# Performance work log

Measured on AMD Instinct MI355X. Metric: run time of the kernel, lower is better.

Reference implementation:

```python
import jax, jax.numpy as jnp
import numpy as np

N_DRUG = 25000
N_DIS = 25000
N = N_DRUG + N_DIS
E = 800000
D_IN = 128
D_OUT = 128


def setup_inputs() -> dict:
    key = jax.random.key(0)
    k1, k2, k3, k4, k5, k6 = jax.random.split(key, 6)
    drug_f = jax.random.normal(k1, (N_DRUG, D_IN), dtype=jnp.float32)
    disease_f = jax.random.normal(k2, (N_DIS, D_IN), dtype=jnp.float32)
    rows = jax.random.randint(k3, (E,), 0, N, dtype=jnp.int64)
    cols = jax.random.randint(k4, (E,), 0, N, dtype=jnp.int64)
    # xavier_uniform_ equivalent for [D_IN, D_OUT]
    limit = float(np.sqrt(6.0 / (D_IN + D_OUT)))
    drug_w = jax.random.uniform(k5, (D_IN, D_OUT), minval=-limit, maxval=limit, dtype=jnp.float32)
    disease_w = jax.random.uniform(k6, (D_IN, D_OUT), minval=-limit, maxval=limit, dtype=jnp.float32)
    return {"drug_f": drug_f, "disease_f": disease_f, "drug_w": drug_w,
            "disease_w": disease_w, "rows": rows, "cols": cols}


def reference(drug_f, disease_f, drug_w, disease_w, rows, cols):
    # per-type linear projection
    drug_h = drug_f @ drug_w          # [n_drug, D_OUT]
    dis_h = disease_f @ disease_w     # [n_dis,  D_OUT]
    node_f = jnp.concatenate([drug_h, dis_h], axis=0)  # [N, D_OUT]
    # row-sum degrees of the (unit-valued) sparse adjacency, clamped at 1
    deg = jax.ops.segment_sum(jnp.ones((rows.shape[0],), node_f.dtype), rows,
                              num_segments=N)
    norm = jnp.clip(deg, 1.0, None) ** -0.5           # [N]
    # symmetric norm: norm * (A @ (norm * x)); SpMM as gather + segment_sum
    node_f = node_f * norm[:, None]
    msgs = node_f[cols]                               # [E, D_OUT]
    node_f = jax.ops.segment_sum(msgs, rows, num_segments=N)
    node_f = node_f * norm[:, None]
    return node_f
```

## Files before the change

### kernel.cpp

```cpp
#include <hip/hip_runtime.h>
#include <hip/hip_bf16.h>

#define D 128
#define CAP 64
#define BINSH 7
#define NSHARD 8
#define NCHUNK 384

typedef short short8 __attribute__((ext_vector_type(8)));
typedef unsigned short ushort8 __attribute__((ext_vector_type(8)));
typedef float f32x4  __attribute__((ext_vector_type(4)));

__device__ __forceinline__ short f2bf(float x) {
    __hip_bfloat16 b = __float2bfloat16(x);
    return *reinterpret_cast<short*>(&b);
}
__device__ __forceinline__ float bf2f(unsigned short u) {
    return __uint_as_float((unsigned)u << 16);
}

__global__ __launch_bounds__(256) void part_proj_kernel(
    const int* __restrict__ rows, const int* __restrict__ cols,
    int* __restrict__ counts, unsigned int* __restrict__ payload,
    int E, int nbin, int nparts, int pe, int capseg,
    const float* __restrict__ f0, const float* __restrict__ f1,
    const float* __restrict__ w0, const float* __restrict__ w1,
    __hip_bfloat16* __restrict__ h,
    int n0, int n1, int nb0) {

    __shared__ short8 Wl[2048];
    int b = blockIdx.x;
    int t = threadIdx.x;

    if (b < nparts) {
        int* cur = (int*)&Wl[0];
        for (int i = t; i < nbin; i += 256) cur[i] = 0;
        __syncthreads();
        int lo = b * pe;
        int hi = lo + pe; if (hi > E) hi = E;
        for (int i = lo + t; i < hi; i += 256) {
            int r = rows[i];
            int c = cols[i];
            int bn = r >> BINSH;
            int p = atomicAdd(&cur[bn], 1);
            if (p < capseg)
                payload[((size_t)bn * nparts + b) * capseg + p] =
                    ((unsigned)r << 16) | (unsigned)(c & 0xffff);
        }
        __syncthreads();
        for (int i = t; i < nbin; i += 256) {
            int c = cur[i]; if (c > capseg) c = capseg;
            counts[(size_t)i * nparts + b] = c;
        }
        return;
    }

    int pb = b - nparts;
    int type = (pb >= nb0) ? 1 : 0;
    const float* f = type ? f1 : f0;
    const float* W = type ? w1 : w0;
    int lbase = (type ? (pb - nb0) : pb) * 64;
    int nloc  = type ? n1 : n0;
    int goff  = type ? n0 : 0;

    for (int i = t; i < 2048; i += 256) {
        int lane = i & 63, ts = i >> 6;
        int s = ts & 3, tt = ts >> 2;
        int n = tt * 16 + (lane & 15);
        int kbase = s * 32 + (lane >> 4) * 8;
        short8 v;
        #pragma unroll
        for (int j = 0; j < 8; ++j)
            v[j] = f2bf(W[(size_t)(kbase + j) * D + n]);
        Wl[i] = v;
    }
    __syncthreads();

    int wave = t >> 6;
    int lane = t & 63;
    int m  = lane & 15;
    int kg = lane >> 4;
    int wrow = lbase + wave * 16;

    int arow = wrow + m;
    int arc = (arow < nloc) ? arow : (nloc - 1);
    const float* fr = f + (size_t)arc * D + kg * 8;
    short8 A[4];
    #pragma unroll
    for (int s = 0; s < 4; ++s) {
        float4 x = *(const float4*)(fr + s * 32);
        float4 y = *(const float4*)(fr + s * 32 + 4);
        short8 a;
        a[0] = f2bf(x.x); a[1] = f2bf(x.y); a[2] = f2bf(x.z); a[3] = f2bf(x.w);
        a[4] = f2bf(y.x); a[5] = f2bf(y.y); a[6] = f2bf(y.z); a[7] = f2bf(y.w);
        A[s] = a;
    }

    #pragma unroll
    for (int tt = 0; tt < 8; ++tt) {
        f32x4 acc = {0.f, 0.f, 0.f, 0.f};
        #pragma unroll
        for (int s = 0; s < 4; ++s)
            acc = __builtin_amdgcn_mfma_f32_16x16x32_bf16(A[s], Wl[(tt * 4 + s) * 64 + lane], acc, 0, 0, 0);
        #pragma unroll
        for (int r = 0; r < 4; ++r) {
            int grow = wrow + kg * 4 + r;
            if (grow < nloc)
                h[(size_t)(goff + grow) * D + tt * 16 + m] = __float2bfloat16(acc[r]);
        }
    }
}

__global__ __launch_bounds__(256) void binfill_kernel(const unsigned int* __restrict__ payload,
                                                      const int* __restrict__ counts,
                                                      unsigned short* __restrict__ bucket,
                                                      int* __restrict__ cnt,
                                                      float* __restrict__ normf,
                                                      int nparts, int capseg, int N) {
    __shared__ int rc[128];
    int b = blockIdx.x;
    int t = threadIdx.x;
    if (t < 128) rc[t] = 0;
    __syncthreads();
    if (t < nparts) {
        int cntc = counts[(size_t)b * nparts + t];
        if (cntc > capseg) cntc = capseg;
        const unsigned int* seg = payload + ((size_t)b * nparts + t) * capseg;
        for (int p = 0; p < cntc; ++p) {
            unsigned pay = seg[p];
            int rl = (pay >> 16) & 127;
            int q = atomicAdd(&rc[rl], 1);
            if (q < CAP)
                bucket[(size_t)((b << BINSH) | rl) * CAP + q] = (unsigned short)(pay & 0xffff);
        }
    }
    __syncthreads();
    if (t < 128) {
        int r = (b << BINSH) | t;
        if (r < N) {
            int c = rc[t];
            cnt[r] = c;
            normf[r] = rsqrtf((float)(c < 1 ? 1 : c));
        }
    }
}

__global__ __launch_bounds__(256) void agg_kernel(const int* __restrict__ cnt,
                                                  const float* __restrict__ normf,
                                                  const unsigned short* __restrict__ bucket,
                                                  const __hip_bfloat16* __restrict__ h,
                                                  float* __restrict__ out, int n) {
    int wave = threadIdx.x >> 6;
    int lane = threadIdx.x & 63;
    int r = blockIdx.x * 4 + wave;
    if (r >= n) return;
    int d = cnt[r]; if (d > CAP) d = CAP;
    int s = r * CAP;

    int col = (int)bucket[s + lane];
    int cs  = (lane < d) ? col : 0;
    float wl = (lane < d) ? normf[cs] : 0.f;

    int g  = lane >> 4;
    int sl = lane & 15;

    float acc[8] = {0.f,0.f,0.f,0.f,0.f,0.f,0.f,0.f};
    int j = 0;
    for (; j + 16 <= d; j += 16) {
        int e0 = j + g, e1 = j + 4 + g, e2 = j + 8 + g, e3 = j + 12 + g;
        float w0 = __shfl(wl, e0), w1 = __shfl(wl, e1), w2 = __shfl(wl, e2), w3 = __shfl(wl, e3);
        int   c0 = __shfl(cs, e0), c1 = __shfl(cs, e1), c2 = __shfl(cs, e2), c3 = __shfl(cs, e3);
        ushort8 v0 = *(const ushort8*)&h[(size_t)c0 * D + sl * 8];
        ushort8 v1 = *(const ushort8*)&h[(size_t)c1 * D + sl * 8];
        ushort8 v2 = *(const ushort8*)&h[(size_t)c2 * D + sl * 8];
        ushort8 v3 = *(const ushort8*)&h[(size_t)c3 * D + sl * 8];
        #pragma unroll
        for (int k = 0; k < 8; ++k)
            acc[k] += (w0 * bf2f(v0[k]) + w1 * bf2f(v1[k])) + (w2 * bf2f(v2[k]) + w3 * bf2f(v3[k]));
    }
    for (; j + 8 <= d; j += 8) {
        int e0 = j + g, e1 = j + 4 + g;
        float w0 = __shfl(wl, e0), w1 = __shfl(wl, e1);
        int   c0 = __shfl(cs, e0), c1 = __shfl(cs, e1);
        ushort8 v0 = *(const ushort8*)&h[(size_t)c0 * D + sl * 8];
        ushort8 v1 = *(const ushort8*)&h[(size_t)c1 * D + sl * 8];
        #pragma unroll
        for (int k = 0; k < 8; ++k)
            acc[k] += w0 * bf2f(v0[k]) + w1 * bf2f(v1[k]);
    }
    for (; j < d; j += 4) {
        int e = j + g;
        float we = __shfl(wl, e & 63); if (e >= d) we = 0.f;
        int   ce = __shfl(cs, e & 63);
        ushort8 v = *(const ushort8*)&h[(size_t)ce * D + sl * 8];
        #pragma unroll
        for (int k = 0; k < 8; ++k)
            acc[k] += we * bf2f(v[k]);
    }
    #pragma unroll
    for (int k = 0; k < 8; ++k) {
        acc[k] += __shfl_xor(acc[k], 16);
        acc[k] += __shfl_xor(acc[k], 32);
    }
    if (g == 0) {
        float nr = normf[r];
        float* po = &out[(size_t)r * D + sl * 8];
        *(float4*)po       = make_float4(acc[0]*nr, acc[1]*nr, acc[2]*nr, acc[3]*nr);
        *(float4*)(po + 4) = make_float4(acc[4]*nr, acc[5]*nr, acc[6]*nr, acc[7]*nr);
    }
}

__global__ void zero_cnt_kernel(int* __restrict__ cnt, int N) {
    int i = blockIdx.x * 256 + threadIdx.x;
    if (i < N) cnt[i] = 0;
}

__global__ __launch_bounds__(256) void fill_shard_kernel(const int* __restrict__ rows,
                                                         const int* __restrict__ cols,
                                                         int* __restrict__ cnt,
                                                         unsigned short* __restrict__ bucket,
                                                         int E, int shsz, int ch) {
    int s     = blockIdx.x & (NSHARD - 1);
    int chunk = blockIdx.x >> 3;
    int lo = chunk * ch;
    int hi = lo + ch; if (hi > E) hi = E;
    int rlo = s * shsz;
    for (int i = lo + (int)threadIdx.x; i < hi; i += 256) {
        int r = rows[i];
        if ((unsigned)(r - rlo) < (unsigned)shsz) {
            int p = atomicAdd(&cnt[r], 1);
            if (p < CAP) bucket[(size_t)r * CAP + p] = (unsigned short)cols[i];
        }
    }
}

__global__ void norm_from_cnt_kernel(const int* __restrict__ cnt, float* __restrict__ normf, int N) {
    int i = blockIdx.x * 256 + threadIdx.x;
    if (i < N) { int c = cnt[i]; normf[i] = rsqrtf((float)(c < 1 ? 1 : c)); }
}

extern "C" void kernel_launch(void* const* d_in, const int* in_sizes, int n_in,
                              void* d_out, int out_size, void* d_ws, size_t ws_size,
                              hipStream_t stream) {
    const float* drug_f    = (const float*)d_in[0];
    const float* disease_f = (const float*)d_in[1];
    const float* drug_w    = (const float*)d_in[2];
    const float* disease_w = (const float*)d_in[3];
    const int*   rows      = (const int*)d_in[4];
    const int*   cols      = (const int*)d_in[5];
    float* out = (float*)d_out;

    int n_drug = in_sizes[0] / D;
    int n_dis  = in_sizes[1] / D;
    int N = n_drug + n_dis;
    int E = in_sizes[4];
    (void)out_size; (void)n_in;

    char* ws = (char*)d_ws;
    size_t off = 0;
    auto alloc = [&](size_t bytes) { void* p = ws + off; off = (off + bytes + 255) & ~(size_t)255; return p; };

    int*            cnt      = (int*)alloc(sizeof(int) * N);
    float*          normf    = (float*)alloc(sizeof(float) * N);
    __hip_bfloat16* h_raw    = (__hip_bfloat16*)alloc(sizeof(__hip_bfloat16) * (size_t)N * D);
    unsigned short* bucket   = (unsigned short*)alloc((size_t)N * CAP * sizeof(unsigned short));

    int nb0 = (n_drug + 63) / 64;
    int nb1 = (n_dis + 63) / 64;

    int nbin = (N + (1 << BINSH) - 1) >> BINSH;
    int pe = (E + 255) / 256;
    if (pe < 4096) pe = 4096;
    int nparts = (E + pe - 1) / pe;
    int capseg = ((pe / nbin) * 3 + 31) & ~15;

    size_t sort_need = off
        + ((sizeof(int) * (size_t)nbin * nparts + 255) & ~(size_t)255)
        + ((sizeof(unsigned int) * (size_t)nbin * nparts * capseg + 255) & ~(size_t)255);

    if (ws_size >= sort_need && nbin <= 512 && nparts <= 256) {
        int*          counts  = (int*)alloc(sizeof(int) * (size_t)nbin * nparts);
        unsigned int* payload = (unsigned int*)alloc(sizeof(unsigned int) * (size_t)nbin * nparts * capseg);

        part_proj_kernel<<<nparts + nb0 + nb1, 256, 0, stream>>>(
            rows, cols, counts, payload, E, nbin, nparts, pe, capseg,
            drug_f, disease_f, drug_w, disease_w, h_raw, n_drug, n_dis, nb0);
        binfill_kernel<<<nbin, 256, 0, stream>>>(payload, counts, bucket, cnt, normf,
                                                 nparts, capseg, N);
        agg_kernel<<<(N + 3) / 4, 256, 0, stream>>>(cnt, normf, bucket, h_raw, out, N);
    } else {
        int shsz = (N + NSHARD - 1) / NSHARD;
        int ch   = (E + NCHUNK - 1) / NCHUNK;

        zero_cnt_kernel<<<(N + 255) / 256, 256, 0, stream>>>(cnt, N);
        fill_shard_kernel<<<NCHUNK * NSHARD, 256, 0, stream>>>(rows, cols, cnt, bucket, E, shsz, ch);
        norm_from_cnt_kernel<<<(N + 255) / 256, 256, 0, stream>>>(cnt, normf, N);
        part_proj_kernel<<<nb0 + nb1, 256, 0, stream>>>(
            rows, cols, (int*)nullptr, (unsigned int*)nullptr, E, nbin, 0, pe, capseg,
            drug_f, disease_f, drug_w, disease_w, h_raw, n_drug, n_dis, nb0);
        agg_kernel<<<(N + 3) / 4, 256, 0, stream>>>(cnt, normf, bucket, h_raw, out, N);
    }
}
```

Before: 64.15 us.

## Replace capped per-bin payload segments with exact local counting sort per partition

Each partition block now builds a histogram of row bins in shared memory, prefix-scans it, scatters the packed (row,col) pairs into a shared staging buffer in bin order, and writes them out contiguously with vectorized stores. It also records per-bin offsets. binfill then reads exact [start,end) ranges instead of fixed-capacity segments. This removes the capseg overflow truncation and the sparse, oversized payload layout, and makes global writes coalesced. The cost is an extra pass over rows plus a block-wide scan in each partition block.

```diff
diff --git a/kernel.cpp b/kernel.cpp
--- a/kernel.cpp
+++ b/kernel.cpp
@@ -4,6 +4,7 @@
 #define D 128
 #define CAP 64
 #define BINSH 7
+#define PE 4096
 #define NSHARD 8
 #define NCHUNK 384
 
@@ -21,8 +22,9 @@
 
 __global__ __launch_bounds__(256) void part_proj_kernel(
     const int* __restrict__ rows, const int* __restrict__ cols,
-    int* __restrict__ counts, unsigned int* __restrict__ payload,
-    int E, int nbin, int nparts, int pe, int capseg,
+    int* __restrict__ base_m,
+    unsigned int* __restrict__ payload,
+    int E, int nbin, int nparts,
     const float* __restrict__ f0, const float* __restrict__ f1,
     const float* __restrict__ w0, const float* __restrict__ w1,
     __hip_bfloat16* __restrict__ h,
@@ -33,25 +35,51 @@
     int t = threadIdx.x;
 
     if (b < nparts) {
-        int* cur = (int*)&Wl[0];
-        for (int i = t; i < nbin; i += 256) cur[i] = 0;
-        __syncthreads();
-        int lo = b * pe;
-        int hi = lo + pe; if (hi > E) hi = E;
+        int* hist = (int*)&Wl[0];
+        int* base = hist + 512;
+        unsigned* staged = (unsigned*)(base + 512);
+        int* sc = (int*)staged;
+
+        int lo = b * PE;
+        int hi = lo + PE; if (hi > E) hi = E;
+        int npe = hi - lo;
+
+        for (int i = t; i < 512; i += 256) hist[i] = 0;
+        __syncthreads();
+        for (int i = lo + t; i < hi; i += 256)
+            atomicAdd(&hist[rows[i] >> BINSH], 1);
+        __syncthreads();
+        int h0 = hist[2 * t], h1 = hist[2 * t + 1];
+        int psum = h0 + h1;
+        sc[t] = psum;
+        __syncthreads();
+        for (int off = 1; off < 256; off <<= 1) {
+            int v = (t >= off) ? sc[t - off] : 0;
+            __syncthreads();
+            sc[t] += v;
+            __syncthreads();
+        }
+        int b0 = sc[t] - psum;
+        base[2 * t]     = b0;
+        base[2 * t + 1] = b0 + h0;
+        __syncthreads();
+        int* brow = base_m + (size_t)b * (nbin + 1);
+        for (int i = t; i < nbin; i += 256) brow[i] = base[i];
+        if (t == 0) brow[nbin] = npe;
+        __syncthreads();
         for (int i = lo + t; i < hi; i += 256) {
             int r = rows[i];
             int c = cols[i];
-            int bn = r >> BINSH;
-            int p = atomicAdd(&cur[bn], 1);
-            if (p < capseg)
-                payload[((size_t)bn * nparts + b) * capseg + p] =
-                    ((unsigned)r << 16) | (unsigned)(c & 0xffff);
-        }
-        __syncthreads();
-        for (int i = t; i < nbin; i += 256) {
-            int c = cur[i]; if (c > capseg) c = capseg;
-            counts[(size_t)i * nparts + b] = c;
-        }
+            int slot = atomicAdd(&base[r >> BINSH], 1);
+            staged[slot] = ((unsigned)r << 16) | (unsigned)(c & 0xffff);
+        }
+        __syncthreads();
+        unsigned* dst = payload + (size_t)b * PE;
+        int nv = npe & ~3;
+        for (int i = t * 4; i + 3 < nv + 4 && i + 3 < npe + 4; i += 1024) {
+            if (i + 3 < nv) *(uint4*)(dst + i) = *(const uint4*)(staged + i);
+        }
+        for (int i = nv + t; i < npe; i += 256) dst[i] = staged[i];
         return;
     }
 
@@ -112,22 +140,22 @@
 }
 
 __global__ __launch_bounds__(256) void binfill_kernel(const unsigned int* __restrict__ payload,
-                                                      const int* __restrict__ counts,
+                                                      const int* __restrict__ base_m,
                                                       unsigned short* __restrict__ bucket,
                                                       int* __restrict__ cnt,
                                                       float* __restrict__ normf,
-                                                      int nparts, int capseg, int N) {
+                                                      int nparts, int nbin, int N) {
     __shared__ int rc[128];
     int b = blockIdx.x;
     int t = threadIdx.x;
     if (t < 128) rc[t] = 0;
     __syncthreads();
     if (t < nparts) {
-        int cntc = counts[(size_t)b * nparts + t];
-        if (cntc > capseg) cntc = capseg;
-        const unsigned int* seg = payload + ((size_t)b * nparts + t) * capseg;
-        for (int p = 0; p < cntc; ++p) {
-            unsigned pay = seg[p];
+        const int* brow = base_m + (size_t)t * (nbin + 1);
+        int s = brow[b], e = brow[b + 1];
+        const unsigned int* src = payload + (size_t)t * PE;
+        for (int p = s; p < e; ++p) {
+            unsigned pay = src[p];
             int rl = (pay >> 16) & 127;
             int q = atomicAdd(&rc[rl], 1);
             if (q < CAP)
@@ -268,25 +296,22 @@
     int nb0 = (n_drug + 63) / 64;
     int nb1 = (n_dis + 63) / 64;
 
-    int nbin = (N + (1 << BINSH) - 1) >> BINSH;
-    int pe = (E + 255) / 256;
-    if (pe < 4096) pe = 4096;
-    int nparts = (E + pe - 1) / pe;
-    int capseg = ((pe / nbin) * 3 + 31) & ~15;
+    int nbin   = (N + (1 << BINSH) - 1) >> BINSH;
+    int nparts = (E + PE - 1) / PE;
 
     size_t sort_need = off
-        + ((sizeof(int) * (size_t)nbin * nparts + 255) & ~(size_t)255)
-        + ((sizeof(unsigned int) * (size_t)nbin * nparts * capseg + 255) & ~(size_t)255);
+        + ((sizeof(int) * (size_t)nparts * (nbin + 1) + 255) & ~(size_t)255)
+        + ((sizeof(unsigned int) * (size_t)nparts * PE + 255) & ~(size_t)255);
 
     if (ws_size >= sort_need && nbin <= 512 && nparts <= 256) {
-        int*          counts  = (int*)alloc(sizeof(int) * (size_t)nbin * nparts);
-        unsigned int* payload = (unsigned int*)alloc(sizeof(unsigned int) * (size_t)nbin * nparts * capseg);
+        int*          base_m  = (int*)alloc(sizeof(int) * (size_t)nparts * (nbin + 1));
+        unsigned int* payload = (unsigned int*)alloc(sizeof(unsigned int) * (size_t)nparts * PE);
 
         part_proj_kernel<<<nparts + nb0 + nb1, 256, 0, stream>>>(
-            rows, cols, counts, payload, E, nbin, nparts, pe, capseg,
+            rows, cols, base_m, payload, E, nbin, nparts,
             drug_f, disease_f, drug_w, disease_w, h_raw, n_drug, n_dis, nb0);
-        binfill_kernel<<<nbin, 256, 0, stream>>>(payload, counts, bucket, cnt, normf,
-                                                 nparts, capseg, N);
+        binfill_kernel<<<nbin, 256, 0, stream>>>(payload, base_m, bucket, cnt, normf,
+                                                 nparts, nbin, N);
         agg_kernel<<<(N + 3) / 4, 256, 0, stream>>>(cnt, normf, bucket, h_raw, out, N);
     } else {
         int shsz = (N + NSHARD - 1) / NSHARD;
@@ -296,7 +321,7 @@
         fill_shard_kernel<<<NCHUNK * NSHARD, 256, 0, stream>>>(rows, cols, cnt, bucket, E, shsz, ch);
         norm_from_cnt_kernel<<<(N + 255) / 256, 256, 0, stream>>>(cnt, normf, N);
         part_proj_kernel<<<nb0 + nb1, 256, 0, stream>>>(
-            rows, cols, (int*)nullptr, (unsigned int*)nullptr, E, nbin, 0, pe, capseg,
+            rows, cols, (int*)nullptr, (unsigned int*)nullptr, E, nbin, 0,
             drug_f, disease_f, drug_w, disease_w, h_raw, n_drug, n_dis, nb0);
         agg_kernel<<<(N + 3) / 4, 256, 0, stream>>>(cnt, normf, bucket, h_raw, out, N);
     }
```

After: 64.38 us. Within noise of the previous version (+0.3%).
